# Kernel tuning notes

Hardware: AMD Instinct MI355X
Metric: run time of the kernel (lower is better)

Reference implementation:

```python
import jax, jax.numpy as jnp
import numpy as np

B, S_IN, T_OUT, H, L, V = 64, 512, 64, 1024, 2, 1024


def setup_inputs() -> dict:
    key = jax.random.key(0)
    ks = iter(jax.random.split(key, 64))
    def p(shape, scale=0.02):
        return (jax.random.normal(next(ks), shape, jnp.float32) * scale)
    d = {"x": jax.random.normal(next(ks), (B, 2, S_IN), jnp.float32)}
    d["emb"] = p((V, H))
    for l in range(L):
        i = 2 if l == 0 else H
        d[f"enc_Wih{l}"] = p((3 * H, i)); d[f"enc_Whh{l}"] = p((3 * H, H))
        d[f"enc_bih{l}"] = p((3 * H,));   d[f"enc_bhh{l}"] = p((3 * H,))
        d[f"dec_Wih{l}"] = p((H, H));     d[f"dec_Whh{l}"] = p((H, H))
        d[f"dec_bih{l}"] = p((H,));       d[f"dec_bhh{l}"] = p((H,))
    d["hq_W"] = p((H, H)); d["hq_b"] = p((H,))
    d["comb_W"] = p((H, 2 * H)); d["comb_b"] = p((H,))
    d["fc_W"] = p((V, H)); d["fc_b"] = p((V,))
    return d


def _gru_layer(x_seq, Wih, Whh, bih, bhh):
    # x_seq: [B,T,I] -> (outputs [B,T,H], h_T [B,H]). PyTorch GRU gate order r,z,n.
    xp = jnp.einsum('bti,gi->btg', x_seq, Wih) + bih  # [B,T,3H]
    h0 = jnp.zeros((x_seq.shape[0], Whh.shape[1]), x_seq.dtype)
    def step(h, xpt):
        hp = h @ Whh.T + bhh
        xr, xz, xn = jnp.split(xpt, 3, axis=-1)
        hr, hz, hn = jnp.split(hp, 3, axis=-1)
        r = jax.nn.sigmoid(xr + hr)
        z = jax.nn.sigmoid(xz + hz)
        n = jnp.tanh(xn + r * hn)
        h = (1.0 - z) * n + z * h
        return h, h
    hT, ys = jax.lax.scan(step, h0, jnp.swapaxes(xp, 0, 1))
    return jnp.swapaxes(ys, 0, 1), hT


def _forward(x, emb,
             enc_Wih0, enc_Whh0, enc_bih0, enc_bhh0,
             enc_Wih1, enc_Whh1, enc_bih1, enc_bhh1,
             dec_Wih0, dec_Whh0, dec_bih0, dec_bhh0,
             dec_Wih1, dec_Whh1, dec_bih1, dec_bhh1,
             hq_W, hq_b, comb_W, comb_b, fc_W, fc_b):
    enc_params = [(enc_Wih0, enc_Whh0, enc_bih0, enc_bhh0),
                  (enc_Wih1, enc_Whh1, enc_bih1, enc_bhh1)]
    dec_params = [(dec_Wih0, dec_Whh0, dec_bih0, dec_bhh0),
                  (dec_Wih1, dec_Whh1, dec_bih1, dec_bhh1)]
    # ---- encoder: GRU over x permuted to [B, S_in, 2] ----
    seq = jnp.transpose(x, (0, 2, 1)).astype(jnp.float32)
    h_enc = []
    for (Wih, Whh, bih, bhh) in enc_params:
        seq, hT = _gru_layer(seq, Wih, Whh, bih, bhh)
        h_enc.append(hT)
    enc_outs = seq                      # [B, S_in, H]
    hidden0 = jnp.stack(h_enc, axis=0)  # [L, B, H]

    tok0 = jnp.zeros((B,), jnp.int32)
    def dec_step(carry, _):
        tok, hid = carry
        inp = emb[tok]                  # [B, H]
        new_h = []
        for l, (Wih, Whh, bih, bhh) in enumerate(dec_params):
            h = jnp.tanh(inp @ Wih.T + bih + hid[l] @ Whh.T + bhh)
            new_h.append(h)
            inp = h
        hid = jnp.stack(new_h, axis=0)
        q = inp @ hq_W.T + hq_b                          # [B, H]
        scores = jnp.einsum('bsh,bh->bs', enc_outs, q)   # [B, S_in]
        aw = jax.nn.softmax(scores, axis=1)
        att = jnp.einsum('bs,bsh->bh', aw, enc_outs)     # [B, H]
        logits = jnp.concatenate([inp, att], axis=-1) @ comb_W.T + comb_b
        logits = logits @ fc_W.T + fc_b                  # [B, V]
        tok = jnp.argmax(logits, axis=-1).astype(jnp.int32)
        return (tok, hid), (logits, aw)
    (_, hidden), (logits_t, aw_t) = jax.lax.scan(dec_step, (tok0, hidden0), None, length=T_OUT)
    vec_out = jnp.swapaxes(logits_t, 0, 1)   # [B, T_out, V]
    attn = aw_t[-1][:, None, :]              # [B, 1, S_in] (last step, as in source)
    return vec_out, hidden, attn


def reference(x, emb,
              enc_Wih0, enc_Whh0, enc_bih0, enc_bhh0,
              enc_Wih1, enc_Whh1, enc_bih1, enc_bhh1,
              dec_Wih0, dec_Whh0, dec_bih0, dec_bhh0,
              dec_Wih1, dec_Whh1, dec_bih1, dec_bhh1,
              hq_W, hq_b, comb_W, comb_b, fc_W, fc_b):
    return _forward(x, emb,
                    enc_Wih0, enc_Whh0, enc_bih0, enc_bhh0,
                    enc_Wih1, enc_Whh1, enc_bih1, enc_bhh1,
                    dec_Wih0, dec_Whh0, dec_bih0, dec_bhh0,
                    dec_Wih1, dec_Whh1, dec_bih1, dec_bhh1,
                    hq_W, hq_b, comb_W, comb_b, fc_W, fc_b)
```

## Files before the change

kernel.cpp:

```cpp
#include <hip/hip_runtime.h>
#include <stdint.h>


#define BB 64
#define SS 512
#define TT 64
#define HH 1024
#define VV 1024
#define BH 65536
#define SH 524288
#define OFF_HID  4194304
#define OFF_ATTN 4325376

typedef _Float16 half8  __attribute__((ext_vector_type(8)));
typedef float    floatx4 __attribute__((ext_vector_type(4)));

struct P {
  const float *x, *emb;
  const float *eWih0, *eWhh0, *ebih0, *ebhh0;
  const float *dWih0, *dWhh0, *dbih0, *dbhh0;
  const float *eWih1, *eWhh1, *ebih1, *ebhh1;
  const float *dWih1, *dWhh1, *dbih1, *dbhh1;
  const float *hqW, *hqb, *combW, *combb, *fcW, *fcb;
  uint32_t* enc_i;
  _Float16 *W0h,*W0l;
  _Float16 *W1h,*W1l;
  _Float16 *embh,*embl,*T0h,*T0l;
  _Float16 *wih0dh,*wih0dl,*wih1dh,*wih1dl,*whh0dh,*whh0dl,*whh1dh,*whh1dl;
  _Float16 *hqh,*hql,*combh,*combl,*fch,*fcl;
  _Float16 *h0h,*h0l,*h1h,*h1l;
  _Float16 *dh0h,*dh0l,*dh1h,*dh1l;
  _Float16 *cath,*catl;
  _Float16 *ch,*cl;
  float *u0,*u1,*w1x,*q;
  float *attp_o;
  float *attp_ml;
  float *sc63;
  unsigned long long* amax;
  float* dout;
};

struct GSet { const _Float16 *Wh, *Wl, *Ah, *Al; const float *bias; float *out; };

__device__ __forceinline__ void splitf(float x, _Float16& hi, _Float16& lo){
  _Float16 h = (_Float16)x; hi = h;
  lo = (_Float16)((x - (float)h) * 2048.0f);
}
__device__ __forceinline__ float reconf(_Float16 hi, _Float16 lo){
  return fmaf((float)lo, 1.0f/2048.0f, (float)hi);
}
__device__ __forceinline__ float recon_u32(uint32_t w){
  float hi = (float)__builtin_bit_cast(_Float16, (unsigned short)(w & 0xffffu));
  float lo = (float)__builtin_bit_cast(_Float16, (unsigned short)(w >> 16));
  return fmaf(lo, 1.0f/2048.0f, hi);
}
__device__ __forceinline__ uint32_t pack_pair(float x){
  _Float16 hi, lo; splitf(x, hi, lo);
  return (uint32_t)__builtin_bit_cast(unsigned short, hi)
       | ((uint32_t)__builtin_bit_cast(unsigned short, lo) << 16);
}
__device__ __forceinline__ unsigned ordf(float f){
  unsigned u = __float_as_uint(f);
  return (u & 0x80000000u) ? ~u : (u | 0x80000000u);
}

template<int NT, int KH, bool SPLIT>
__device__ __forceinline__ void gemm_core(
    const _Float16* __restrict__ Ah0, const _Float16* __restrict__ Al0,
    const _Float16* __restrict__ Ah1, const _Float16* __restrict__ Al1,
    int sA,
    const _Float16* __restrict__ Wh, const _Float16* __restrict__ Wl,
    int nrows, _Float16* ldsW, float* accOut)
{
  const int tid = threadIdx.x, lane = tid & 63, wave = tid >> 6;
  const int mA = (wave<<4) + (lane & 15);
  const int kb = ((lane>>4) << 3);
  const int wstride = KH << 10;
  floatx4 aH[NT], aM1[NT], aM2[NT];
  int ne[NT];
  const _Float16* bh_base[NT];
  const _Float16* bl_base[NT];
  #pragma unroll
  for (int nt=0; nt<NT; ++nt){
    int nn = (lane & 15) + (nt<<4);
    ne[nt] = nn < nrows ? nn : nrows - 1;
    bh_base[nt] = ldsW + ne[nt]*1032 + kb;
    aH[nt]  = floatx4{0.f,0.f,0.f,0.f};
    aM1[nt] = floatx4{0.f,0.f,0.f,0.f};
    aM2[nt] = floatx4{0.f,0.f,0.f,0.f};
  }
  #pragma unroll
  for (int kh=0; kh<KH; ++kh){
    __syncthreads();
    const int iters = (nrows*128 + 255) >> 8;
    for (int it=0; it<iters; ++it){
      int idx = tid + (it<<8);
      int row = idx >> 7, col = (idx & 127) << 3;
      if (row < nrows)
        *(half8*)(ldsW + row*1032 + col) =
            *(const half8*)(Wh + row*wstride + (kh<<10) + col);
    }
    __syncthreads();
    const _Float16* ah_p = ((KH==2 && kh==1) ? Ah1 : Ah0) + mA*sA + kb;
    const _Float16* al_p = ((KH==2 && kh==1) ? Al1 : Al0) + mA*sA + kb;
    #pragma unroll
    for (int nt=0; nt<NT; ++nt) bl_base[nt] = Wl + ne[nt]*wstride + (kh<<10) + kb;
    #pragma unroll 4
    for (int ks=0; ks<32; ++ks){
      half8 ah = *(const half8*)(ah_p + (ks<<5));
      half8 al = *(const half8*)(al_p + (ks<<5));
      #pragma unroll
      for (int nt=0; nt<NT; ++nt){
        half8 bh = *(const half8*)(bh_base[nt] + (ks<<5));
        half8 bl = *(const half8*)(bl_base[nt] + (ks<<5));
        aH[nt]  = __builtin_amdgcn_mfma_f32_16x16x32_f16(ah, bh, aH[nt],  0,0,0);
        aM1[nt] = __builtin_amdgcn_mfma_f32_16x16x32_f16(ah, bl, aM1[nt], 0,0,0);
        aM2[nt] = __builtin_amdgcn_mfma_f32_16x16x32_f16(al, bh, aM2[nt], 0,0,0);
      }
    }
    if (SPLIT){
      #pragma unroll
      for (int nt=0; nt<NT; ++nt){
        #pragma unroll
        for (int r=0;r<4;++r)
          accOut[(kh*NT + nt)*4 + r] = aH[nt][r] + (aM1[nt][r] + aM2[nt][r]) * (1.f/2048.f);
        aH[nt]  = floatx4{0.f,0.f,0.f,0.f};
        aM1[nt] = floatx4{0.f,0.f,0.f,0.f};
        aM2[nt] = floatx4{0.f,0.f,0.f,0.f};
      }
    }
  }
  if (!SPLIT){
    #pragma unroll
    for (int nt=0; nt<NT; ++nt)
      #pragma unroll
      for (int r=0;r<4;++r)
        accOut[nt*4 + r] = aH[nt][r] + (aM1[nt][r] + aM2[nt][r]) * (1.f/2048.f);
  }
}

__global__ __launch_bounds__(256) void k_split(const float* __restrict__ src,
                                               _Float16* dh, _Float16* dl, int n){
  for (int i = blockIdx.x*256 + threadIdx.x; i < n; i += gridDim.x*256){
    _Float16 hi,lo; splitf(src[i],hi,lo); dh[i]=hi; dl[i]=lo;
  }
}

__global__ __launch_bounds__(256) void k_rw0(P p){
  const int n = 256*12*1024;
  for (int i = blockIdx.x*256 + threadIdx.x; i < n; i += gridDim.x*256){
    int k = i & 1023; int rest = i >> 10; int rr = rest % 12; int blk = rest / 12;
    int grow = (rr>>2)*1024 + (blk<<2) + (rr&3);
    _Float16 hi,lo; splitf(p.eWhh0[grow*1024 + k],hi,lo);
    p.W0h[i]=hi; p.W0l[i]=lo;
  }
}
__global__ __launch_bounds__(256) void k_rw1(P p){
  const int n = 256*12*2048;
  for (int i = blockIdx.x*256 + threadIdx.x; i < n; i += gridDim.x*256){
    int k = i & 2047; int rest = i >> 11; int rr = rest % 12; int blk = rest / 12;
    int grow = (rr>>2)*1024 + (blk<<2) + (rr&3);
    float v = (k < 1024) ? p.eWhh1[grow*1024 + k] : p.eWih1[grow*1024 + (k-1024)];
    _Float16 hi,lo; splitf(v,hi,lo);
    p.W1h[i]=hi; p.W1l[i]=lo;
  }
}
__global__ __launch_bounds__(256) void k_zero(P p){
  int i = blockIdx.x*256 + threadIdx.x;
  p.h1h[i] = (_Float16)0.f; p.h1l[i] = (_Float16)0.f;
  p.h0h[BH + i] = (_Float16)0.f; p.h0l[BH + i] = (_Float16)0.f;
}
__global__ __launch_bounds__(256) void k_t0(P p){
  __shared__ _Float16 ldsW[16*1032];
  const int ns = blockIdx.x & 63, mc = blockIdx.x >> 6;
  float acc[4];
  gemm_core<1,1,false>(p.embh + mc*65536, p.embl + mc*65536, nullptr, nullptr, 1024,
                       p.wih0dh + ns*16*1024, p.wih0dl + ns*16*1024, 16, ldsW, acc);
  const int lane = threadIdx.x & 63, wave = threadIdx.x >> 6;
  const int n = lane & 15, col = (ns<<4) + n;
  const float bv = p.dbih0[col];
  #pragma unroll
  for (int r=0;r<4;++r){
    int v = mc*64 + (wave<<4) + ((lane>>4)<<2) + r;
    _Float16 hi,lo; splitf(acc[r] + bv, hi, lo);
    p.T0h[v*1024 + col] = hi; p.T0l[v*1024 + col] = lo;
  }
}

__global__ __launch_bounds__(256,2) void k_enc(P p, int e){
  __shared__ _Float16 ldsW[24768];
  __shared__ float ldsG[2*12*68];
  __shared__ float ldsC[12*4];
  const int tid = threadIdx.x, lane = tid & 63, wave = tid >> 6;
  const bool is0 = blockIdx.x < 256;
  if (is0 && e >= 512) return;
  if (!is0 && e < 1) return;
  const int blk = is0 ? (int)blockIdx.x : (int)blockIdx.x - 256;
  const int j0 = blk << 2;

  if (is0){
    const _Float16* gh = p.W0h + blk*12*1024;
    const _Float16* gl = p.W0l + blk*12*1024;
    _Float16* Wl = ldsW + 12*1032;
    for (int it = tid; it < 12*128; it += 256){
      int row = it >> 7, col = (it & 127) << 3;
      *(half8*)(ldsW + row*1032 + col) = *(const half8*)(gh + row*1024 + col);
      *(half8*)(Wl   + row*1032 + col) = *(const half8*)(gl + row*1024 + col);
    }
  } else {
    const _Float16* gh = p.W1h + blk*12*2048;
    for (int it = tid; it < 12*256; it += 256){
      int row = it >> 8, col = (it & 255) << 3;
      *(half8*)(ldsW + row*2056 + col) = *(const half8*)(gh + row*2048 + col);
    }
  }
  if (tid < 12){
    int grow = (tid>>2)*1024 + j0 + (tid & 3);
    if (is0){
      ldsC[tid*4+0] = p.eWih0[grow*2+0];
      ldsC[tid*4+1] = p.eWih0[grow*2+1];
      ldsC[tid*4+2] = p.ebih0[grow];
      ldsC[tid*4+3] = p.ebhh0[grow];
    } else {
      ldsC[tid*4+0] = p.ebih1[grow];
      ldsC[tid*4+1] = p.ebhh1[grow];
    }
  }
  __syncthreads();

  const int cur = e & 1, prv = cur ^ 1;
  const int mA = (wave<<4) + (lane & 15);
  const int kb = ((lane>>4) << 3);
  const int nn = lane & 15;
  const int ne = nn < 12 ? nn : 11;
  const int b_ep = tid & 63, c_ep = tid >> 6;
  const int col_ep = j0 + c_ep;

  if (is0){
    floatx4 aH{0.f,0.f,0.f,0.f}, aM1{0.f,0.f,0.f,0.f}, aM2{0.f,0.f,0.f,0.f};
    const _Float16* ah_p = p.h0h + prv*BH + mA*1024 + kb;
    const _Float16* al_p = p.h0l + prv*BH + mA*1024 + kb;
    const _Float16* bh_p = ldsW + ne*1032 + kb;
    const _Float16* bl_p = ldsW + 12*1032 + ne*1032 + kb;
    #pragma unroll 4
    for (int ks=0; ks<32; ++ks){
      half8 ah = *(const half8*)(ah_p + (ks<<5));
      half8 al = *(const half8*)(al_p + (ks<<5));
      half8 bh = *(const half8*)(bh_p + (ks<<5));
      half8 bl = *(const half8*)(bl_p + (ks<<5));
      aH  = __builtin_amdgcn_mfma_f32_16x16x32_f16(ah, bh, aH,  0,0,0);
      aM1 = __builtin_amdgcn_mfma_f32_16x16x32_f16(ah, bl, aM1, 0,0,0);
      aM2 = __builtin_amdgcn_mfma_f32_16x16x32_f16(al, bh, aM2, 0,0,0);
    }
    if (nn < 12){
      #pragma unroll
      for (int r=0;r<4;++r)
        ldsG[nn*68 + (wave<<4)+((lane>>4)<<2)+r] =
            aH[r] + (aM1[r] + aM2[r]) * (1.f/2048.f);
    }
    __syncthreads();
    {
      const int b = b_ep, c = c_ep, col = col_ep;
      float hr = ldsG[c*68+b]     + ldsC[c*4+3];
      float hz = ldsG[(4+c)*68+b] + ldsC[(4+c)*4+3];
      float hn = ldsG[(8+c)*68+b] + ldsC[(8+c)*4+3];
      float x0 = p.x[b*1024 + e], x1 = p.x[b*1024 + 512 + e];
      float xr = fmaf(x0, ldsC[c*4+0],     fmaf(x1, ldsC[c*4+1],     ldsC[c*4+2]));
      float xz = fmaf(x0, ldsC[(4+c)*4+0], fmaf(x1, ldsC[(4+c)*4+1], ldsC[(4+c)*4+2]));
      float xn = fmaf(x0, ldsC[(8+c)*4+0], fmaf(x1, ldsC[(8+c)*4+1], ldsC[(8+c)*4+2]));
      float rg = 1.0f/(1.0f + expf(-(xr+hr)));
      float zg = 1.0f/(1.0f + expf(-(xz+hz)));
      float ng = tanhf(xn + rg*hn);
      float hold = reconf(p.h0h[prv*BH + b*1024 + col], p.h0l[prv*BH + b*1024 + col]);
      float hnew = (1.0f - zg)*ng + zg*hold;
      _Float16 hi,lo; splitf(hnew,hi,lo);
      p.h0h[cur*BH + b*1024 + col] = hi;
      p.h0l[cur*BH + b*1024 + col] = lo;
    }
  } else {
    #pragma unroll
    for (int kh=0; kh<2; ++kh){
      floatx4 aH{0.f,0.f,0.f,0.f}, aM1{0.f,0.f,0.f,0.f}, aM2{0.f,0.f,0.f,0.f};
      const _Float16* ah_p = (kh ? p.h0h : p.h1h) + prv*BH + mA*1024 + kb;
      const _Float16* al_p = (kh ? p.h0l : p.h1l) + prv*BH + mA*1024 + kb;
      const _Float16* bh_p = ldsW + ne*2056 + (kh<<10) + kb;
      const _Float16* bl_p = p.W1l + blk*12*2048 + ne*2048 + (kh<<10) + kb;
      #pragma unroll 4
      for (int ks=0; ks<32; ++ks){
        half8 ah = *(const half8*)(ah_p + (ks<<5));
        half8 al = *(const half8*)(al_p + (ks<<5));
        half8 bh = *(const half8*)(bh_p + (ks<<5));
        half8 bl = *(const half8*)(bl_p + (ks<<5));
        aH  = __builtin_amdgcn_mfma_f32_16x16x32_f16(ah, bh, aH,  0,0,0);
        aM1 = __builtin_amdgcn_mfma_f32_16x16x32_f16(ah, bl, aM1, 0,0,0);
        aM2 = __builtin_amdgcn_mfma_f32_16x16x32_f16(al, bh, aM2, 0,0,0);
      }
      if (nn < 12){
        #pragma unroll
        for (int r=0;r<4;++r)
          ldsG[(kh*12+nn)*68 + (wave<<4)+((lane>>4)<<2)+r] =
              aH[r] + (aM1[r] + aM2[r]) * (1.f/2048.f);
      }
    }
    __syncthreads();
    {
      const int b = b_ep, c = c_ep, col = col_ep;
      const int t = e - 1;
      float hr = ldsG[c*68+b]        + ldsC[c*4+1];
      float hz = ldsG[(4+c)*68+b]    + ldsC[(4+c)*4+1];
      float hn = ldsG[(8+c)*68+b]    + ldsC[(8+c)*4+1];
      float xr = ldsG[(12+c)*68+b]   + ldsC[c*4+0];
      float xz = ldsG[(12+4+c)*68+b] + ldsC[(4+c)*4+0];
      float xn = ldsG[(12+8+c)*68+b] + ldsC[(8+c)*4+0];
      float rg = 1.0f/(1.0f + expf(-(xr+hr)));
      float zg = 1.0f/(1.0f + expf(-(xz+hz)));
      float ng = tanhf(xn + rg*hn);
      float hold = reconf(p.h1h[prv*BH + b*1024 + col], p.h1l[prv*BH + b*1024 + col]);
      float hnew = (1.0f - zg)*ng + zg*hold;
      _Float16 hi,lo; splitf(hnew,hi,lo);
      p.h1h[cur*BH + b*1024 + col] = hi;
      p.h1l[cur*BH + b*1024 + col] = lo;
      p.enc_i[b*SH + t*1024 + col] = pack_pair(hnew);
    }
  }
}

__global__ __launch_bounds__(256) void k_dgemm2(GSet a, GSet b){
  const int tid = threadIdx.x, lane = tid & 63, wave = tid >> 6;
  const GSet g = blockIdx.x < 128 ? a : b;
  const int blk = blockIdx.x & 127;
  __shared__ _Float16 ldsW[8*1032];
  float acc[4];
  gemm_core<1,1,false>(g.Ah, g.Al, nullptr, nullptr, 1024,
                       g.Wh + blk*8*1024, g.Wl + blk*8*1024, 8, ldsW, acc);
  int n = lane & 15;
  if (n < 8){
    int col = (blk<<3) + n;
    float bv = g.bias[col];
    #pragma unroll
    for (int r=0;r<4;++r){
      int m = (wave<<4)+((lane>>4)<<2)+r;
      g.out[m*1024 + col] = acc[r] + bv;
    }
  }
}

__global__ __launch_bounds__(256) void k_dec0(P p, int t){
  const int tid = threadIdx.x, b = blockIdx.x;
  __shared__ unsigned long long red[256];
  unsigned long long v = 0;
  if (t > 0 && tid < 128) v = p.amax[b*128 + tid];
  red[tid] = v; __syncthreads();
  for (int off=128; off>=1; off>>=1){
    if (tid < off){ unsigned long long o = red[tid+off]; if (o > red[tid]) red[tid] = o; }
    __syncthreads();
  }
  const int tokb = (t > 0) ? (1023 - (int)(red[0] & 0xffffffffULL)) : 0;
  #pragma unroll
  for (int i=0;i<4;++i){
    int h = tid + (i<<8);
    float val = tanhf(reconf(p.T0h[tokb*1024+h], p.T0l[tokb*1024+h]) + p.u0[b*1024+h]);
    _Float16 hi,lo; splitf(val,hi,lo);
    p.dh0h[b*1024+h]=hi; p.dh0l[b*1024+h]=lo;
  }
}
__global__ __launch_bounds__(256) void k_dec2(P p){
  const int tid = threadIdx.x, b = blockIdx.x;
  #pragma unroll
  for (int i=0;i<4;++i){
    int h = tid + (i<<8);
    float val = tanhf(p.w1x[b*1024+h] + p.u1[b*1024+h]);
    _Float16 hi,lo; splitf(val,hi,lo);
    p.dh1h[b*1024+h]=hi; p.dh1l[b*1024+h]=lo;
    p.cath[b*2048+h]=hi; p.catl[b*2048+h]=lo;
  }
}
__global__ __launch_bounds__(256) void k_flash(P p, int t){
  const int tid = threadIdx.x, lane = tid & 63, wave = tid >> 6;
  const int b = blockIdx.x >> 1, half = blockIdx.x & 1;
  const int s0 = half << 8;
  const bool last = (t == 63);
  float qv[16];
  #pragma unroll
  for (int i=0;i<16;++i) qv[i] = p.q[b*1024 + (i<<6) + lane];
  float ov[16];
  #pragma unroll
  for (int i=0;i<16;++i) ov[i] = 0.f;
  float mrun = -3.0e38f, lrun = 0.f;
  for (int si=0; si<64; ++si){
    int s = s0 + (wave<<6) + si;
    const uint32_t* ep = p.enc_i + b*SH + s*1024 + lane;
    float ef[16]; float partial = 0.f;
    #pragma unroll
    for (int i=0;i<16;++i){
      ef[i] = recon_u32(ep[i<<6]);
      partial = fmaf(ef[i], qv[i], partial);
    }
    #pragma unroll
    for (int off=32; off; off>>=1) partial += __shfl_xor(partial, off, 64);
    if (last && lane == 0) p.sc63[b*512 + s] = partial;
    float mnew = fmaxf(mrun, partial);
    float fac = __expf(mrun - mnew);
    float w   = __expf(partial - mnew);
    lrun = fmaf(lrun, fac, w);
    #pragma unroll
    for (int i=0;i<16;++i) ov[i] = fmaf(ov[i], fac, w*ef[i]);
    mrun = mnew;
  }
  __shared__ float ldsO[4][1024];
  __shared__ float ldsM[4], ldsL2[4];
  #pragma unroll
  for (int i=0;i<16;++i) ldsO[wave][(i<<6)+lane] = ov[i];
  if (lane == 0){ ldsM[wave] = mrun; ldsL2[wave] = lrun; }
  __syncthreads();
  float M = fmaxf(fmaxf(ldsM[0],ldsM[1]), fmaxf(ldsM[2],ldsM[3]));
  float f0 = __expf(ldsM[0]-M), f1 = __expf(ldsM[1]-M),
        f2 = __expf(ldsM[2]-M), f3 = __expf(ldsM[3]-M);
  if (tid == 0){
    p.attp_ml[b*4 + half*2 + 0] = M;
    p.attp_ml[b*4 + half*2 + 1] = f0*ldsL2[0] + f1*ldsL2[1] + f2*ldsL2[2] + f3*ldsL2[3];
  }
  #pragma unroll
  for (int i=0;i<4;++i){
    int h = tid + (i<<8);
    p.attp_o[(b*2+half)*1024 + h] =
        f0*ldsO[0][h] + f1*ldsO[1][h] + f2*ldsO[2][h] + f3*ldsO[3][h];
  }
}
__global__ __launch_bounds__(256) void k_dec5(P p, int t){
  const int tid = threadIdx.x, b = blockIdx.x;
  float m0 = p.attp_ml[b*4+0], l0 = p.attp_ml[b*4+1];
  float m1 = p.attp_ml[b*4+2], l1 = p.attp_ml[b*4+3];
  float M = fmaxf(m0,m1);
  float f0 = expf(m0-M), f1 = expf(m1-M);
  float invL = 1.0f/(f0*l0 + f1*l1);
  #pragma unroll
  for (int i=0;i<4;++i){
    int h = tid + (i<<8);
    float o = (f0*p.attp_o[(b*2+0)*1024+h] + f1*p.attp_o[(b*2+1)*1024+h]) * invL;
    _Float16 hi,lo; splitf(o,hi,lo);
    p.cath[b*2048 + 1024 + h] = hi; p.catl[b*2048 + 1024 + h] = lo;
  }
  if (t == 63){
    #pragma unroll
    for (int i=0;i<2;++i){
      int s = tid + (i<<8);
      p.dout[OFF_ATTN + b*512 + s] = expf(p.sc63[b*512+s] - M) * invL;
    }
  }
}
__global__ __launch_bounds__(256) void k_comb(P p){
  const int tid = threadIdx.x, lane = tid & 63, wave = tid >> 6;
  const int blk = blockIdx.x;
  __shared__ _Float16 ldsW[8*1032];
  float acc[4];
  gemm_core<1,2,false>(p.cath, p.catl, p.cath + 1024, p.catl + 1024, 2048,
                       p.combh + blk*8*2048, p.combl + blk*8*2048, 8, ldsW, acc);
  int n = lane & 15;
  if (n < 8){
    int col = (blk<<3) + n;
    float bv = p.combb[col];
    #pragma unroll
    for (int r=0;r<4;++r){
      int m = (wave<<4)+((lane>>4)<<2)+r;
      _Float16 hi,lo; splitf(acc[r] + bv, hi, lo);
      p.ch[m*1024 + col] = hi; p.cl[m*1024 + col] = lo;
    }
  }
}
__global__ __launch_bounds__(256) void k_fc(P p, int t){
  const int tid = threadIdx.x, lane = tid & 63, wave = tid >> 6;
  const int blk = blockIdx.x;
  __shared__ _Float16 ldsW[8*1032];
  __shared__ float ldsL[8][68];
  float acc[4];
  gemm_core<1,1,false>(p.ch, p.cl, nullptr, nullptr, 1024,
                       p.fch + blk*8*1024, p.fcl + blk*8*1024, 8, ldsW, acc);
  int n = lane & 15;
  if (n < 8){
    int col = (blk<<3) + n;
    float bv = p.fcb[col];
    #pragma unroll
    for (int r=0;r<4;++r){
      int m = (wave<<4)+((lane>>4)<<2)+r;
      float val = acc[r] + bv;
      p.dout[m*65536 + t*1024 + col] = val;
      ldsL[n][m] = val;
    }
  }
  __syncthreads();
  if (tid < 64){
    int b = tid; float best = -3.0e38f; int bi = 0;
    #pragma unroll
    for (int jj=0; jj<8; ++jj){
      float v = ldsL[jj][b];
      if (v > best){ best = v; bi = jj; }
    }
    unsigned long long pk = ((unsigned long long)ordf(best) << 32)
                          | (unsigned)(1023 - ((blk<<3) + bi));
    p.amax[b*128 + blk] = pk;
  }
}
__global__ __launch_bounds__(256) void k_hidden(P p){
  int idx = blockIdx.x*256 + threadIdx.x;
  int i = idx & 65535;
  float v = (idx >> 16) ? reconf(p.dh1h[i], p.dh1l[i]) : reconf(p.dh0h[i], p.dh0l[i]);
  p.dout[OFF_HID + idx] = v;
}

extern "C" void kernel_launch(void* const* d_in, const int* in_sizes, int n_in,
                              void* d_out, int out_size, void* d_ws, size_t ws_size,
                              hipStream_t stream)
{
  (void)in_sizes; (void)n_in; (void)out_size;
  P p;
  p.x     = (const float*)d_in[0];  p.emb   = (const float*)d_in[1];
  p.eWih0 = (const float*)d_in[2];  p.eWhh0 = (const float*)d_in[3];
  p.ebih0 = (const float*)d_in[4];  p.ebhh0 = (const float*)d_in[5];
  p.dWih0 = (const float*)d_in[6];  p.dWhh0 = (const float*)d_in[7];
  p.dbih0 = (const float*)d_in[8];  p.dbhh0 = (const float*)d_in[9];
  p.eWih1 = (const float*)d_in[10]; p.eWhh1 = (const float*)d_in[11];
  p.ebih1 = (const float*)d_in[12]; p.ebhh1 = (const float*)d_in[13];
  p.dWih1 = (const float*)d_in[14]; p.dWhh1 = (const float*)d_in[15];
  p.dbih1 = (const float*)d_in[16]; p.dbhh1 = (const float*)d_in[17];
  p.hqW   = (const float*)d_in[18]; p.hqb   = (const float*)d_in[19];
  p.combW = (const float*)d_in[20]; p.combb = (const float*)d_in[21];
  p.fcW   = (const float*)d_in[22]; p.fcb   = (const float*)d_in[23];
  p.dout  = (float*)d_out;

  char* base = (char*)d_ws; size_t off = 0;
  auto alloc = [&](size_t bytes)->char*{
    char* r = base + off; off = (off + bytes + 255) & ~(size_t)255; return r;
  };
  p.enc_i = (uint32_t*)alloc(33554432ULL*4);
  p.W0h = (_Float16*)alloc(3145728ULL*2);  p.W0l = (_Float16*)alloc(3145728ULL*2);
  p.W1h = (_Float16*)alloc(6291456ULL*2);  p.W1l = (_Float16*)alloc(6291456ULL*2);
  p.embh = (_Float16*)alloc(1048576ULL*2); p.embl = (_Float16*)alloc(1048576ULL*2);
  p.T0h  = (_Float16*)alloc(1048576ULL*2); p.T0l  = (_Float16*)alloc(1048576ULL*2);
  p.wih0dh=(_Float16*)alloc(1048576ULL*2); p.wih0dl=(_Float16*)alloc(1048576ULL*2);
  p.wih1dh=(_Float16*)alloc(1048576ULL*2); p.wih1dl=(_Float16*)alloc(1048576ULL*2);
  p.whh0dh=(_Float16*)alloc(1048576ULL*2); p.whh0dl=(_Float16*)alloc(1048576ULL*2);
  p.whh1dh=(_Float16*)alloc(1048576ULL*2); p.whh1dl=(_Float16*)alloc(1048576ULL*2);
  p.hqh  = (_Float16*)alloc(1048576ULL*2); p.hql  = (_Float16*)alloc(1048576ULL*2);
  p.combh= (_Float16*)alloc(2097152ULL*2); p.combl= (_Float16*)alloc(2097152ULL*2);
  p.fch  = (_Float16*)alloc(1048576ULL*2); p.fcl  = (_Float16*)alloc(1048576ULL*2);
  p.h0h  = (_Float16*)alloc(131072ULL*2);  p.h0l  = (_Float16*)alloc(131072ULL*2);
  p.h1h  = (_Float16*)alloc(131072ULL*2);  p.h1l  = (_Float16*)alloc(131072ULL*2);
  p.dh0h = (_Float16*)alloc(65536ULL*2);   p.dh0l = (_Float16*)alloc(65536ULL*2);
  p.dh1h = (_Float16*)alloc(65536ULL*2);   p.dh1l = (_Float16*)alloc(65536ULL*2);
  p.cath = (_Float16*)alloc(131072ULL*2);  p.catl = (_Float16*)alloc(131072ULL*2);
  p.ch   = (_Float16*)alloc(65536ULL*2);   p.cl   = (_Float16*)alloc(65536ULL*2);
  p.u0   = (float*)alloc(65536ULL*4);      p.u1   = (float*)alloc(65536ULL*4);
  p.w1x  = (float*)alloc(65536ULL*4);      p.q    = (float*)alloc(65536ULL*4);
  p.attp_o  = (float*)alloc(131072ULL*4);
  p.attp_ml = (float*)alloc(256ULL*4);
  p.sc63    = (float*)alloc(32768ULL*4);
  p.amax    = (unsigned long long*)alloc(8192ULL*8);
  if (off > ws_size) return;

  k_split<<<2048,256,0,stream>>>(p.emb,   p.embh,   p.embl,   1048576);
  k_split<<<2048,256,0,stream>>>(p.dWih0, p.wih0dh, p.wih0dl, 1048576);
  k_split<<<2048,256,0,stream>>>(p.dWih1, p.wih1dh, p.wih1dl, 1048576);
  k_split<<<2048,256,0,stream>>>(p.dWhh0, p.whh0dh, p.whh0dl, 1048576);
  k_split<<<2048,256,0,stream>>>(p.dWhh1, p.whh1dh, p.whh1dl, 1048576);
  k_split<<<2048,256,0,stream>>>(p.hqW,   p.hqh,    p.hql,    1048576);
  k_split<<<2048,256,0,stream>>>(p.combW, p.combh,  p.combl,  2097152);
  k_split<<<2048,256,0,stream>>>(p.fcW,   p.fch,    p.fcl,    1048576);
  k_rw0<<<4096,256,0,stream>>>(p);
  k_rw1<<<4096,256,0,stream>>>(p);
  k_zero<<<256,256,0,stream>>>(p);
  k_t0<<<1024,256,0,stream>>>(p);

  for (int e=0; e<=512; ++e) k_enc<<<512,256,0,stream>>>(p, e);

  {
    GSet a{p.whh0dh, p.whh0dl, p.h0h + BH, p.h0l + BH, p.dbhh0, p.u0};
    GSet b{p.whh1dh, p.whh1dl, p.h1h,      p.h1l,      p.dbhh1, p.u1};
    k_dgemm2<<<256,256,0,stream>>>(a, b);
  }
  GSet sK1a{p.wih1dh, p.wih1dl, p.dh0h, p.dh0l, p.dbih1, p.w1x};
  GSet sK1b{p.whh0dh, p.whh0dl, p.dh0h, p.dh0l, p.dbhh0, p.u0};
  GSet sK3a{p.hqh,    p.hql,    p.dh1h, p.dh1l, p.hqb,   p.q};
  GSet sK3b{p.whh1dh, p.whh1dl, p.dh1h, p.dh1l, p.dbhh1, p.u1};

  for (int t=0; t<64; ++t){
    k_dec0<<<64,256,0,stream>>>(p, t);
    k_dgemm2<<<256,256,0,stream>>>(sK1a, sK1b);
    k_dec2<<<64,256,0,stream>>>(p);
    k_dgemm2<<<256,256,0,stream>>>(sK3a, sK3b);
    k_flash<<<128,256,0,stream>>>(p, t);
    k_dec5<<<64,256,0,stream>>>(p, t);
    k_comb<<<128,256,0,stream>>>(p);
    k_fc<<<128,256,0,stream>>>(p, t);
  }
  k_hidden<<<512,256,0,stream>>>(p);
}
```

Baseline: 28.65 ms.

## Fuse decoder tanh into GEMM epilogue and merge flash attention halves

The tanh/split step that built the layer-1 decoder hidden state now runs in the epilogue of the first dual GEMM, so the separate elementwise kernel and the w1x round trip through global memory are gone. The flash attention kernel now handles all 512 source positions of a batch row in one 512-thread block. It does the softmax merge and output normalisation in shared memory, which replaces the separate reduction kernel and its partial-result buffers. This removes two launches per decoder step, but the attention pass now runs on half as many blocks, which may cut the memory parallelism available to that stage.

After: 28.68 ms (median of 2 runs). About the same (+0.1%).

```diff
diff --git a/kernel.cpp b/kernel.cpp
--- a/kernel.cpp
+++ b/kernel.cpp
@@ -33,9 +33,6 @@
   _Float16 *cath,*catl;
   _Float16 *ch,*cl;
   float *u0,*u1,*w1x,*q;
-  float *attp_o;
-  float *attp_ml;
-  float *sc63;
   unsigned long long* amax;
   float* dout;
 };
@@ -345,6 +342,38 @@
   }
 }
 
+__global__ __launch_bounds__(256) void k_dgemm2h1(P p, GSet a, GSet b){
+  const int tid = threadIdx.x, lane = tid & 63, wave = tid >> 6;
+  const bool isa = blockIdx.x < 128;
+  const GSet g = isa ? a : b;
+  const int blk = blockIdx.x & 127;
+  __shared__ _Float16 ldsW[8*1032];
+  float acc[4];
+  gemm_core<1,1,false>(g.Ah, g.Al, nullptr, nullptr, 1024,
+                       g.Wh + blk*8*1024, g.Wl + blk*8*1024, 8, ldsW, acc);
+  int n = lane & 15;
+  if (n < 8){
+    int col = (blk<<3) + n;
+    float bv = g.bias[col];
+    if (isa){
+      #pragma unroll
+      for (int r=0;r<4;++r){
+        int m = (wave<<4)+((lane>>4)<<2)+r;
+        float val = tanhf((acc[r] + bv) + p.u1[m*1024 + col]);
+        _Float16 hi,lo; splitf(val,hi,lo);
+        p.dh1h[m*1024+col]=hi; p.dh1l[m*1024+col]=lo;
+        p.cath[m*2048+col]=hi; p.catl[m*2048+col]=lo;
+      }
+    } else {
+      #pragma unroll
+      for (int r=0;r<4;++r){
+        int m = (wave<<4)+((lane>>4)<<2)+r;
+        g.out[m*1024 + col] = acc[r] + bv;
+      }
+    }
+  }
+}
+
 __global__ __launch_bounds__(256) void k_dec0(P p, int t){
   const int tid = threadIdx.x, b = blockIdx.x;
   __shared__ unsigned long long red[256];
@@ -364,21 +393,9 @@
     p.dh0h[b*1024+h]=hi; p.dh0l[b*1024+h]=lo;
   }
 }
-__global__ __launch_bounds__(256) void k_dec2(P p){
-  const int tid = threadIdx.x, b = blockIdx.x;
-  #pragma unroll
-  for (int i=0;i<4;++i){
-    int h = tid + (i<<8);
-    float val = tanhf(p.w1x[b*1024+h] + p.u1[b*1024+h]);
-    _Float16 hi,lo; splitf(val,hi,lo);
-    p.dh1h[b*1024+h]=hi; p.dh1l[b*1024+h]=lo;
-    p.cath[b*2048+h]=hi; p.catl[b*2048+h]=lo;
-  }
-}
-__global__ __launch_bounds__(256) void k_flash(P p, int t){
-  const int tid = threadIdx.x, lane = tid & 63, wave = tid >> 6;
-  const int b = blockIdx.x >> 1, half = blockIdx.x & 1;
-  const int s0 = half << 8;
+__global__ __launch_bounds__(512) void k_flash8(P p, int t){
+  const int tid = threadIdx.x, lane = tid & 63, wave = tid >> 6;
+  const int b = blockIdx.x;
   const bool last = (t == 63);
   float qv[16];
   #pragma unroll
@@ -386,9 +403,12 @@
   float ov[16];
   #pragma unroll
   for (int i=0;i<16;++i) ov[i] = 0.f;
+  __shared__ float ldsO[8][1024];
+  __shared__ float ldsM[8], ldsL2[8];
+  __shared__ float ldsS[512];
   float mrun = -3.0e38f, lrun = 0.f;
   for (int si=0; si<64; ++si){
-    int s = s0 + (wave<<6) + si;
+    int s = (wave<<6) + si;
     const uint32_t* ep = p.enc_i + b*SH + s*1024 + lane;
     float ef[16]; float partial = 0.f;
     #pragma unroll
@@ -398,7 +418,7 @@
     }
     #pragma unroll
     for (int off=32; off; off>>=1) partial += __shfl_xor(partial, off, 64);
-    if (last && lane == 0) p.sc63[b*512 + s] = partial;
+    if (last && lane == 0) ldsS[s] = partial;
     float mnew = fmaxf(mrun, partial);
     float fac = __expf(mrun - mnew);
     float w   = __expf(partial - mnew);
@@ -407,46 +427,33 @@
     for (int i=0;i<16;++i) ov[i] = fmaf(ov[i], fac, w*ef[i]);
     mrun = mnew;
   }
-  __shared__ float ldsO[4][1024];
-  __shared__ float ldsM[4], ldsL2[4];
   #pragma unroll
   for (int i=0;i<16;++i) ldsO[wave][(i<<6)+lane] = ov[i];
   if (lane == 0){ ldsM[wave] = mrun; ldsL2[wave] = lrun; }
   __syncthreads();
-  float M = fmaxf(fmaxf(ldsM[0],ldsM[1]), fmaxf(ldsM[2],ldsM[3]));
-  float f0 = __expf(ldsM[0]-M), f1 = __expf(ldsM[1]-M),
-        f2 = __expf(ldsM[2]-M), f3 = __expf(ldsM[3]-M);
-  if (tid == 0){
-    p.attp_ml[b*4 + half*2 + 0] = M;
-    p.attp_ml[b*4 + half*2 + 1] = f0*ldsL2[0] + f1*ldsL2[1] + f2*ldsL2[2] + f3*ldsL2[3];
-  }
-  #pragma unroll
-  for (int i=0;i<4;++i){
-    int h = tid + (i<<8);
-    p.attp_o[(b*2+half)*1024 + h] =
-        f0*ldsO[0][h] + f1*ldsO[1][h] + f2*ldsO[2][h] + f3*ldsO[3][h];
-  }
-}
-__global__ __launch_bounds__(256) void k_dec5(P p, int t){
-  const int tid = threadIdx.x, b = blockIdx.x;
-  float m0 = p.attp_ml[b*4+0], l0 = p.attp_ml[b*4+1];
-  float m1 = p.attp_ml[b*4+2], l1 = p.attp_ml[b*4+3];
-  float M = fmaxf(m0,m1);
-  float f0 = expf(m0-M), f1 = expf(m1-M);
-  float invL = 1.0f/(f0*l0 + f1*l1);
-  #pragma unroll
-  for (int i=0;i<4;++i){
-    int h = tid + (i<<8);
-    float o = (f0*p.attp_o[(b*2+0)*1024+h] + f1*p.attp_o[(b*2+1)*1024+h]) * invL;
+  float M0 = fmaxf(fmaxf(ldsM[0],ldsM[1]), fmaxf(ldsM[2],ldsM[3]));
+  float g0 = __expf(ldsM[0]-M0), g1 = __expf(ldsM[1]-M0),
+        g2 = __expf(ldsM[2]-M0), g3 = __expf(ldsM[3]-M0);
+  float lH0 = g0*ldsL2[0] + g1*ldsL2[1] + g2*ldsL2[2] + g3*ldsL2[3];
+  float M1 = fmaxf(fmaxf(ldsM[4],ldsM[5]), fmaxf(ldsM[6],ldsM[7]));
+  float g4 = __expf(ldsM[4]-M1), g5 = __expf(ldsM[5]-M1),
+        g6 = __expf(ldsM[6]-M1), g7 = __expf(ldsM[7]-M1);
+  float lH1 = g4*ldsL2[4] + g5*ldsL2[5] + g6*ldsL2[6] + g7*ldsL2[7];
+  float M = fmaxf(M0,M1);
+  float F0 = expf(M0-M), F1 = expf(M1-M);
+  float invL = 1.0f/(F0*lH0 + F1*lH1);
+  #pragma unroll
+  for (int i=0;i<2;++i){
+    int h = tid + (i<<9);
+    float a0 = g0*ldsO[0][h] + g1*ldsO[1][h] + g2*ldsO[2][h] + g3*ldsO[3][h];
+    float a1 = g4*ldsO[4][h] + g5*ldsO[5][h] + g6*ldsO[6][h] + g7*ldsO[7][h];
+    float o = (F0*a0 + F1*a1) * invL;
     _Float16 hi,lo; splitf(o,hi,lo);
     p.cath[b*2048 + 1024 + h] = hi; p.catl[b*2048 + 1024 + h] = lo;
   }
-  if (t == 63){
-    #pragma unroll
-    for (int i=0;i<2;++i){
-      int s = tid + (i<<8);
-      p.dout[OFF_ATTN + b*512 + s] = expf(p.sc63[b*512+s] - M) * invL;
-    }
+  if (last){
+    int s = tid;
+    p.dout[OFF_ATTN + b*512 + s] = expf(ldsS[s] - M) * invL;
   }
 }
 __global__ __launch_bounds__(256) void k_comb(P p){
@@ -552,9 +559,6 @@
   p.ch   = (_Float16*)alloc(65536ULL*2);   p.cl   = (_Float16*)alloc(65536ULL*2);
   p.u0   = (float*)alloc(65536ULL*4);      p.u1   = (float*)alloc(65536ULL*4);
   p.w1x  = (float*)alloc(65536ULL*4);      p.q    = (float*)alloc(65536ULL*4);
-  p.attp_o  = (float*)alloc(131072ULL*4);
-  p.attp_ml = (float*)alloc(256ULL*4);
-  p.sc63    = (float*)alloc(32768ULL*4);
   p.amax    = (unsigned long long*)alloc(8192ULL*8);
   if (off > ws_size) return;
 
@@ -585,11 +589,9 @@
 
   for (int t=0; t<64; ++t){
     k_dec0<<<64,256,0,stream>>>(p, t);
-    k_dgemm2<<<256,256,0,stream>>>(sK1a, sK1b);
-    k_dec2<<<64,256,0,stream>>>(p);
+    k_dgemm2h1<<<256,256,0,stream>>>(p, sK1a, sK1b);
     k_dgemm2<<<256,256,0,stream>>>(sK3a, sK3b);
-    k_flash<<<128,256,0,stream>>>(p, t);
-    k_dec5<<<64,256,0,stream>>>(p, t);
+    k_flash8<<<64,512,0,stream>>>(p, t);
     k_comb<<<128,256,0,stream>>>(p);
     k_fc<<<128,256,0,stream>>>(p, t);
   }
```
